# Performance work log

Measured on AMD Instinct MI355X. Metric: run time of the kernel, lower is better.

Reference implementation:

```python
import jax, jax.numpy as jnp
import numpy as np

B, F, S = 64, 128, 2048
K_LIST = [8, 4, 2]  # c**i for i in range(k,0,-1) with k=3, c=2
EPS = 1e-5


def setup_inputs() -> dict:
    key = jax.random.key(0)
    ks = jax.random.split(key, 16)
    d = {}
    d["x"] = jax.random.normal(ks[0], (B, F, S), dtype=jnp.float32)
    # BatchNorm1d(seq_len*feature_num) affine params (train-mode batch stats)
    d["bn_gamma"] = jnp.ones((F * S,), jnp.float32)
    d["bn_beta"] = jnp.zeros((F * S,), jnp.float32)
    i = 1
    for s, k in enumerate(K_LIST):
        L = S // k
        d[f"selw1_{s}"] = (jax.random.normal(ks[i], (3 * F, 64), jnp.float32) / np.sqrt(3 * F)).astype(jnp.float32); i += 1
        d[f"selb1_{s}"] = jnp.zeros((64,), jnp.float32)
        d[f"selw2_{s}"] = (jax.random.normal(ks[i], (64, 1), jnp.float32) / 8.0).astype(jnp.float32); i += 1
        d[f"selb2_{s}"] = jnp.zeros((1,), jnp.float32)
        d[f"linw1_{s}"] = (jax.random.normal(ks[i], (L, L), jnp.float32) / np.sqrt(L)).astype(jnp.float32); i += 1
        d[f"linb1_{s}"] = jnp.zeros((L,), jnp.float32)
        d[f"linw2_{s}"] = (jax.random.normal(ks[i], (L, 2 * L), jnp.float32) / np.sqrt(L)).astype(jnp.float32); i += 1
        d[f"linb2_{s}"] = jnp.zeros((2 * L,), jnp.float32)
    return d


def _forward(x, bn_gamma, bn_beta, sel, lin):
    Bx, Fx, Sx = x.shape
    # BatchNorm1d over flattened [B, F*S] channels, training-mode batch stats (biased var)
    xf = x.reshape(Bx, -1)
    mu = xf.mean(axis=0)
    var = xf.var(axis=0)
    xf = (xf - mu) * jax.lax.rsqrt(var + EPS) * bn_gamma + bn_beta
    x = xf.reshape(Bx, Fx, Sx)

    samples = []
    for s, k in enumerate(K_LIST):
        L = Sx // k
        xr = x.reshape(Bx, Fx, L, k)           # non-overlapping windows (kernel==stride)
        avg = xr.mean(axis=-1)                 # AvgPool1d  [B, F, L]
        mx = xr.max(axis=-1)                   # MaxPool1d  [B, F, L]
        pfs = 0.5 * (avg + mx)
        stats = jnp.concatenate(
            [pfs.mean(axis=-1), pfs.std(axis=-1, ddof=1), pfs.max(axis=-1)], axis=1
        )                                      # [B, 3F]
        w1, b1, w2, b2 = sel[s]
        w = jax.nn.sigmoid(jax.nn.relu(stats @ w1 + b1) @ w2 + b2)  # [B, 1] (dropout is eval/identity)
        w = w[:, :, None]                      # [B, 1, 1]
        samples.append(w * avg + (1.0 - w) * mx)
    samples.append(x)

    for s in range(len(K_LIST)):
        lw1, lb1, lw2, lb2 = lin[s]
        h = jax.nn.gelu(samples[s] @ lw1 + lb1, approximate=False)
        samples[s + 1] = samples[s + 1] + h @ lw2 + lb2
    return samples[-1]


def reference(x, bn_gamma, bn_beta,
              selw1_0, selb1_0, selw2_0, selb2_0, linw1_0, linb1_0, linw2_0, linb2_0,
              selw1_1, selb1_1, selw2_1, selb2_1, linw1_1, linb1_1, linw2_1, linb2_1,
              selw1_2, selb1_2, selw2_2, selb2_2, linw1_2, linb1_2, linw2_2, linb2_2):
    sel = [(selw1_0, selb1_0, selw2_0, selb2_0),
           (selw1_1, selb1_1, selw2_1, selb2_1),
           (selw1_2, selb1_2, selw2_2, selb2_2)]
    lin = [(linw1_0, linb1_0, linw2_0, linb2_0),
           (linw1_1, linb1_1, linw2_1, linb2_1),
           (linw1_2, linb1_2, linw2_2, linb2_2)]
    return _forward(x, bn_gamma, bn_beta, sel, lin)
```

## Files before the change

kernel.cpp:

```cpp
#include <hip/hip_runtime.h>
#include <hip/hip_bf16.h>
#include <math.h>

#define B_ 64
#define F_ 128
#define S_ 2048
#define FS_ (F_*S_)
#define M_  (B_*F_)
#define EPS_ 1e-5f

typedef __bf16 v8bf __attribute__((ext_vector_type(8)));
typedef float  v4f  __attribute__((ext_vector_type(4)));

__device__ __forceinline__ unsigned short f2bf_rne(float f) {
  unsigned int u = __float_as_uint(f);
  u += 0x7FFF + ((u >> 16) & 1);
  return (unsigned short)(u >> 16);
}

__device__ __forceinline__ float gelu_exact(float x) {
  return 0.5f * x * (1.0f + erff(x * 0.70710678118654752f));
}

#define GLDS16(g, l) __builtin_amdgcn_global_load_lds( \
    (const __attribute__((address_space(1))) unsigned int*)(g), \
    (__attribute__((address_space(3))) unsigned int*)(l), 16, 0, 0)

__global__ __launch_bounds__(256) void bn_stats_k(const float* __restrict__ x,
    const float* __restrict__ gamma, const float* __restrict__ beta,
    float* __restrict__ scl, float* __restrict__ shf)
{
  int j4 = blockIdx.x * 256 + threadIdx.x;
  const float4* x4 = (const float4*)x;
  float sum[4] = {0,0,0,0}, sq[4] = {0,0,0,0};
  for (int b = 0; b < B_; b++) {
    float4 v = x4[(size_t)b * (FS_/4) + j4];
    float vv[4] = {v.x, v.y, v.z, v.w};
    #pragma unroll
    for (int i = 0; i < 4; i++) { sum[i] += vv[i]; sq[i] += vv[i]*vv[i]; }
  }
  #pragma unroll
  for (int i = 0; i < 4; i++) {
    int j = j4*4 + i;
    float mu  = sum[i] * (1.0f/B_);
    float var = sq[i] * (1.0f/B_) - mu*mu;
    float rstd = rsqrtf(var + EPS_);
    float g = gamma[j];
    scl[j] = rstd * g;
    shf[j] = beta[j] - mu * rstd * g;
  }
}

__global__ __launch_bounds__(256) void bnpool_k(const float* __restrict__ x,
    const float* __restrict__ scl, const float* __restrict__ shf,
    float* __restrict__ out, float* __restrict__ stats)
{
  int bf = blockIdx.x, t = threadIdx.x;
  int b = bf >> 7, f = bf & 127;
  const float4* xp  = (const float4*)(x   + (size_t)bf * S_);
  const float4* scp = (const float4*)(scl + (size_t)f  * S_);
  const float4* shp = (const float4*)(shf + (size_t)f  * S_);
  float4* op = (float4*)(out + (size_t)bf * S_);

  float xr[8];
  #pragma unroll
  for (int h = 0; h < 2; h++) {
    int i4 = t*2 + h;
    float4 v = xp[i4], sc = scp[i4], sh = shp[i4];
    float4 o;
    o.x = fmaf(v.x, sc.x, sh.x);
    o.y = fmaf(v.y, sc.y, sh.y);
    o.z = fmaf(v.z, sc.z, sh.z);
    o.w = fmaf(v.w, sc.w, sh.w);
    op[i4] = o;
    xr[h*4+0] = o.x; xr[h*4+1] = o.y; xr[h*4+2] = o.z; xr[h*4+3] = o.w;
  }

  float a2[4], m2[4];
  float ps2 = 0.f, pq2 = 0.f, pm2 = -INFINITY;
  #pragma unroll
  for (int j = 0; j < 4; j++) {
    a2[j] = xr[2*j] + xr[2*j+1];
    m2[j] = fmaxf(xr[2*j], xr[2*j+1]);
    float pf = 0.5f * (0.5f * a2[j] + m2[j]);
    ps2 += pf; pq2 += pf*pf; pm2 = fmaxf(pm2, pf);
  }
  float a4[2], m4[2];
  float ps1 = 0.f, pq1 = 0.f, pm1 = -INFINITY;
  #pragma unroll
  for (int j = 0; j < 2; j++) {
    a4[j] = a2[2*j] + a2[2*j+1];
    m4[j] = fmaxf(m2[2*j], m2[2*j+1]);
    float pf = 0.5f * (0.25f * a4[j] + m4[j]);
    ps1 += pf; pq1 += pf*pf; pm1 = fmaxf(pm1, pf);
  }
  float a8 = a4[0] + a4[1];
  float m8 = fmaxf(m4[0], m4[1]);
  float pf8 = 0.5f * (0.125f * a8 + m8);
  float ps0 = pf8, pq0 = pf8*pf8, pm0 = pf8;

  __shared__ float wred[12];
  int lane = t & 63, wid = t >> 6;
  float PS[3] = {ps0, ps1, ps2}, PQ[3] = {pq0, pq1, pq2}, PM[3] = {pm0, pm1, pm2};
  int   LL[3] = {256, 512, 1024};
  #pragma unroll
  for (int s = 0; s < 3; s++) {
    float vs = PS[s], vq = PQ[s], vm = PM[s];
    #pragma unroll
    for (int off = 32; off > 0; off >>= 1) {
      vs += __shfl_down(vs, off);
      vq += __shfl_down(vq, off);
      vm = fmaxf(vm, __shfl_down(vm, off));
    }
    if (lane == 0) { wred[wid*3+0] = vs; wred[wid*3+1] = vq; wred[wid*3+2] = vm; }
    __syncthreads();
    if (t == 0) {
      float S = 0.f, Q = 0.f, Mx = -INFINITY;
      #pragma unroll
      for (int i = 0; i < 4; i++) {
        S += wred[i*3+0]; Q += wred[i*3+1]; Mx = fmaxf(Mx, wred[i*3+2]);
      }
      float L = (float)LL[s];
      float mean = S / L;
      float var  = (Q - S*S/L) / (L - 1.0f);
      float* base = stats + s*(64*384) + b*384;
      base[f]       = mean;
      base[128 + f] = sqrtf(fmaxf(var, 0.0f));
      base[256 + f] = Mx;
    }
    __syncthreads();
  }
}

__global__ __launch_bounds__(64) void selall_k(const float* __restrict__ stats,
    const float* w1_0, const float* b1_0, const float* w2_0, const float* b2_0,
    const float* w1_1, const float* b1_1, const float* w2_1, const float* b2_1,
    const float* w1_2, const float* b1_2, const float* w2_2, const float* b2_2,
    float* __restrict__ wsel)
{
  int s = blockIdx.y, b = blockIdx.x, j = threadIdx.x;
  const float *w1, *b1, *w2, *b2;
  if      (s == 0) { w1 = w1_0; b1 = b1_0; w2 = w2_0; b2 = b2_0; }
  else if (s == 1) { w1 = w1_1; b1 = b1_1; w2 = w2_1; b2 = b2_1; }
  else             { w1 = w1_2; b1 = b1_2; w2 = w2_2; b2 = b2_2; }
  const float* st = stats + s*(64*384) + b*384;
  float acc = b1[j];
  for (int i = 0; i < 384; i++) acc = fmaf(st[i], w1[i*64 + j], acc);
  float h = fmaxf(acc, 0.0f);
  float v = h * w2[j];
  for (int off = 32; off > 0; off >>= 1) v += __shfl_down(v, off);
  if (j == 0) wsel[s*64 + b] = 1.0f / (1.0f + expf(-(v + b2[0])));
}

__global__ __launch_bounds__(256) void combfused_k(const float* __restrict__ xn,
    const float* __restrict__ wsel,
    unsigned short* __restrict__ o8, unsigned short* __restrict__ o4,
    unsigned short* __restrict__ o2)
{
  int bf = blockIdx.x, t = threadIdx.x, b = bf >> 7;
  float wA = wsel[b];
  float wB = wsel[64 + b];
  float wC = wsel[128 + b];
  const float4* xp = (const float4*)(xn + (size_t)bf * S_);
  float xr[8];
  #pragma unroll
  for (int h = 0; h < 2; h++) {
    float4 v = xp[t*2 + h];
    xr[h*4+0] = v.x; xr[h*4+1] = v.y; xr[h*4+2] = v.z; xr[h*4+3] = v.w;
  }
  float a2[4], m2[4];
  ushort4 u4o;
  unsigned short uu[4];
  #pragma unroll
  for (int j = 0; j < 4; j++) {
    a2[j] = xr[2*j] + xr[2*j+1];
    m2[j] = fmaxf(xr[2*j], xr[2*j+1]);
    uu[j] = f2bf_rne(wC * (0.5f * a2[j]) + (1.0f - wC) * m2[j]);
  }
  u4o.x = uu[0]; u4o.y = uu[1]; u4o.z = uu[2]; u4o.w = uu[3];
  ((ushort4*)(o2 + (size_t)bf * 1024))[t] = u4o;

  float a4[2], m4[2];
  ushort2 u2o;
  #pragma unroll
  for (int j = 0; j < 2; j++) {
    a4[j] = a2[2*j] + a2[2*j+1];
    m4[j] = fmaxf(m2[2*j], m2[2*j+1]);
    unsigned short uv = f2bf_rne(wB * (0.25f * a4[j]) + (1.0f - wB) * m4[j]);
    if (j == 0) u2o.x = uv; else u2o.y = uv;
  }
  ((ushort2*)(o4 + (size_t)bf * 512))[t] = u2o;

  float a8 = a4[0] + a4[1];
  float m8 = fmaxf(m4[0], m4[1]);
  o8[(size_t)bf * 256 + t] = f2bf_rne(wA * (0.125f * a8) + (1.0f - wA) * m8);
}

__global__ __launch_bounds__(256) void wt_all_k(
    const float* w10, unsigned short* t10,
    const float* w20, unsigned short* t20,
    const float* w11, unsigned short* t11,
    const float* w21, unsigned short* t21,
    const float* w12, unsigned short* t12,
    const float* w22, unsigned short* t22)
{
  int bx = blockIdx.x;
  const float* W; unsigned short* T; int K, N, loc;
  if      (bx < 64)   { W = w10; T = t10; K = 256;  N = 256;  loc = bx; }
  else if (bx < 192)  { W = w20; T = t20; K = 256;  N = 512;  loc = bx - 64; }
  else if (bx < 448)  { W = w11; T = t11; K = 512;  N = 512;  loc = bx - 192; }
  else if (bx < 960)  { W = w21; T = t21; K = 512;  N = 1024; loc = bx - 448; }
  else if (bx < 1984) { W = w12; T = t12; K = 1024; N = 1024; loc = bx - 960; }
  else                { W = w22; T = t22; K = 1024; N = 2048; loc = bx - 1984; }
  int nx = N >> 5;
  int k0 = (loc / nx) << 5;
  int n0 = (loc % nx) << 5;
  __shared__ float tile[32][33];
  int tx = threadIdx.x & 31, ty = threadIdx.x >> 5;
  #pragma unroll
  for (int i = ty; i < 32; i += 8)
    tile[i][tx] = W[(size_t)(k0 + i) * N + n0 + tx];
  __syncthreads();
  #pragma unroll
  for (int i = ty; i < 32; i += 8)
    T[(size_t)(n0 + i) * K + k0 + tx] = f2bf_rne(tile[tx][i]);
}

template<int MODE>
__global__ __launch_bounds__(256) void mgemm_k(
    const unsigned short* __restrict__ A,
    const unsigned short* __restrict__ Wt,
    const float* __restrict__ bias,
    const float* ColdF,
    const unsigned short* ColdB,
    unsigned short* Obf,
    float* Of32,
    int K, int N)
{
  __shared__ v8bf As8[128*8];
  __shared__ v8bf Bs8[128*8];
  const int tid  = threadIdx.x;
  const int lane = tid & 63;
  const int w    = tid >> 6;
  const int bm   = blockIdx.y * 128;
  const int bn   = blockIdx.x * 128;
  const int wm   = (w >> 1) * 64;
  const int wn   = (w & 1) * 64;

  v4f acc[4][4];
  #pragma unroll
  for (int i = 0; i < 4; i++)
    #pragma unroll
    for (int j = 0; j < 4; j++)
      acc[i][j] = (v4f){0.f, 0.f, 0.f, 0.f};

  const int lrow = lane >> 3;
  const int lchk = (lane & 7) ^ lrow;
  const unsigned short* ag = A  + (size_t)(bm + w*32 + lrow) * K + lchk * 8;
  const unsigned short* bg = Wt + (size_t)(bn + w*32 + lrow) * K + lchk * 8;
  char* al = (char*)As8 + w*32*128;
  char* bl = (char*)Bs8 + w*32*128;
  const size_t row8 = (size_t)8 * K;

  for (int k0 = 0; k0 < K; k0 += 64) {
    __syncthreads();
    GLDS16(ag + k0,            al);
    GLDS16(ag + row8 + k0,     al + 8*128);
    GLDS16(ag + 2*row8 + k0,   al + 16*128);
    GLDS16(ag + 3*row8 + k0,   al + 24*128);
    GLDS16(bg + k0,            bl);
    GLDS16(bg + row8 + k0,     bl + 8*128);
    GLDS16(bg + 2*row8 + k0,   bl + 16*128);
    GLDS16(bg + 3*row8 + k0,   bl + 24*128);
    __syncthreads();

    #pragma unroll
    for (int u = 0; u < 2; u++) {
      const int cl = (lane >> 4) + u*4;
      const int slot = cl ^ (lane & 7);
      v8bf af[4], bfr[4];
      #pragma unroll
      for (int t = 0; t < 4; t++) {
        af[t]  = As8[(wm + t*16 + (lane & 15))*8 + slot];
        bfr[t] = Bs8[(wn + t*16 + (lane & 15))*8 + slot];
      }
      #pragma unroll
      for (int i = 0; i < 4; i++)
        #pragma unroll
        for (int j = 0; j < 4; j++)
          acc[i][j] = __builtin_amdgcn_mfma_f32_16x16x32_bf16(af[i], bfr[j], acc[i][j], 0, 0, 0);
    }
  }

  const int col0 = bn + wn + (lane & 15);
  const int row0 = bm + wm + ((lane >> 4) << 2);
  #pragma unroll
  for (int j = 0; j < 4; j++) {
    int c = col0 + j*16;
    float bv = bias[c];
    #pragma unroll
    for (int i = 0; i < 4; i++) {
      #pragma unroll
      for (int r = 0; r < 4; r++) {
        int rr = row0 + i*16 + r;
        size_t idx = (size_t)rr * N + c;
        float t = acc[i][j][r] + bv;
        if (MODE == 0) {
          Obf[idx] = f2bf_rne(gelu_exact(t));
        } else if (MODE == 1) {
          float cold = __bfloat162float(*(const __hip_bfloat16*)&ColdB[idx]);
          Obf[idx] = f2bf_rne(t + cold);
        } else {
          Of32[idx] = t + ColdF[idx];
        }
      }
    }
  }
}

extern "C" void kernel_launch(void* const* d_in, const int* in_sizes, int n_in,
                              void* d_out, int out_size, void* d_ws, size_t ws_size,
                              hipStream_t stream)
{
  const float* x     = (const float*)d_in[0];
  const float* gamma = (const float*)d_in[1];
  const float* beta  = (const float*)d_in[2];
  float* out = (float*)d_out;
  float* ws  = (float*)d_ws;

  static const int KS[3] = {8, 4, 2};

  size_t off = 0;
  float* scl   = ws + off; off += FS_;
  float* shf   = ws + off; off += FS_;
  float* stats = ws + off; off += 3*64*384;
  float* wsel  = ws + off; off += 256;
  unsigned short* sampb[3];
  sampb[0] = (unsigned short*)(ws + off); off += (size_t)M_ * 256 / 2;
  sampb[1] = (unsigned short*)(ws + off); off += (size_t)M_ * 512 / 2;
  sampb[2] = (unsigned short*)(ws + off); off += (size_t)M_ * 1024 / 2;
  unsigned short* hb = (unsigned short*)(ws + off); off += (size_t)M_ * 2048 / 2;
  unsigned short *wt1[3], *wt2[3];
  for (int s = 0; s < 3; s++) {
    int L = S_ / KS[s];
    wt1[s] = (unsigned short*)(ws + off); off += (size_t)L * L / 2;
    wt2[s] = (unsigned short*)(ws + off); off += (size_t)L * 2 * L / 2;
  }

  wt_all_k<<<4032, 256, 0, stream>>>(
      (const float*)d_in[3 + 0*8 + 4], wt1[0], (const float*)d_in[3 + 0*8 + 6], wt2[0],
      (const float*)d_in[3 + 1*8 + 4], wt1[1], (const float*)d_in[3 + 1*8 + 6], wt2[1],
      (const float*)d_in[3 + 2*8 + 4], wt1[2], (const float*)d_in[3 + 2*8 + 6], wt2[2]);

  bn_stats_k<<<FS_/4/256, 256, 0, stream>>>(x, gamma, beta, scl, shf);
  bnpool_k<<<M_, 256, 0, stream>>>(x, scl, shf, out, stats);
  selall_k<<<dim3(64, 3), 64, 0, stream>>>(stats,
      (const float*)d_in[3+0], (const float*)d_in[4+0], (const float*)d_in[5+0], (const float*)d_in[6+0],
      (const float*)d_in[3+8], (const float*)d_in[4+8], (const float*)d_in[5+8], (const float*)d_in[6+8],
      (const float*)d_in[3+16], (const float*)d_in[4+16], (const float*)d_in[5+16], (const float*)d_in[6+16],
      wsel);
  combfused_k<<<M_, 256, 0, stream>>>(out, wsel, sampb[0], sampb[1], sampb[2]);

  for (int s = 0; s < 3; s++) {
    int L = S_ / KS[s];
    const float* lb1 = (const float*)d_in[3 + 8*s + 5];
    const float* lb2 = (const float*)d_in[3 + 8*s + 7];
    mgemm_k<0><<<dim3(L/128, M_/128), 256, 0, stream>>>(
        sampb[s], wt1[s], lb1, nullptr, nullptr, hb, nullptr, L, L);
    if (s < 2) {
      mgemm_k<1><<<dim3(2*L/128, M_/128), 256, 0, stream>>>(
          hb, wt2[s], lb2, nullptr, sampb[s+1], sampb[s+1], nullptr, L, 2*L);
    } else {
      mgemm_k<2><<<dim3(2*L/128, M_/128), 256, 0, stream>>>(
          hb, wt2[s], lb2, out, nullptr, nullptr, out, L, 2*L);
    }
  }
}
```

Baseline: 412.8 us.

## Store normalized input as bf16 and switch GEMMs to 32x32x16 MFMA tiles

The BN-normalized activation is now written as a bf16 buffer instead of fp32 to the output. The pooling/combine kernel and the final residual GEMM read that buffer, which halves the traffic for the intermediate. The GEMM kernel now uses 32x32x16 bf16 MFMA with a templated M tile (64 for the smaller GEMMs, which gives more blocks) in place of 16x16x32. The risk is that the final residual adds a bf16-rounded x rather than fp32, which lowers accuracy of the output.

```diff
diff --git a/kernel.cpp b/kernel.cpp
--- a/kernel.cpp
+++ b/kernel.cpp
@@ -10,12 +10,18 @@
 #define EPS_ 1e-5f
 
 typedef __bf16 v8bf __attribute__((ext_vector_type(8)));
-typedef float  v4f  __attribute__((ext_vector_type(4)));
+typedef float  v16f __attribute__((ext_vector_type(16)));
 
 __device__ __forceinline__ unsigned short f2bf_rne(float f) {
   unsigned int u = __float_as_uint(f);
   u += 0x7FFF + ((u >> 16) & 1);
   return (unsigned short)(u >> 16);
+}
+__device__ __forceinline__ float b2f(unsigned short u) {
+  return __uint_as_float(((unsigned int)u) << 16);
+}
+__device__ __forceinline__ unsigned int pack2(float a, float b) {
+  return (unsigned int)f2bf_rne(a) | ((unsigned int)f2bf_rne(b) << 16);
 }
 
 __device__ __forceinline__ float gelu_exact(float x) {
@@ -53,28 +59,28 @@
 
 __global__ __launch_bounds__(256) void bnpool_k(const float* __restrict__ x,
     const float* __restrict__ scl, const float* __restrict__ shf,
-    float* __restrict__ out, float* __restrict__ stats)
+    unsigned short* __restrict__ xnb, float* __restrict__ stats)
 {
   int bf = blockIdx.x, t = threadIdx.x;
   int b = bf >> 7, f = bf & 127;
   const float4* xp  = (const float4*)(x   + (size_t)bf * S_);
   const float4* scp = (const float4*)(scl + (size_t)f  * S_);
   const float4* shp = (const float4*)(shf + (size_t)f  * S_);
-  float4* op = (float4*)(out + (size_t)bf * S_);
 
   float xr[8];
   #pragma unroll
   for (int h = 0; h < 2; h++) {
     int i4 = t*2 + h;
     float4 v = xp[i4], sc = scp[i4], sh = shp[i4];
-    float4 o;
-    o.x = fmaf(v.x, sc.x, sh.x);
-    o.y = fmaf(v.y, sc.y, sh.y);
-    o.z = fmaf(v.z, sc.z, sh.z);
-    o.w = fmaf(v.w, sc.w, sh.w);
-    op[i4] = o;
-    xr[h*4+0] = o.x; xr[h*4+1] = o.y; xr[h*4+2] = o.z; xr[h*4+3] = o.w;
-  }
+    xr[h*4+0] = fmaf(v.x, sc.x, sh.x);
+    xr[h*4+1] = fmaf(v.y, sc.y, sh.y);
+    xr[h*4+2] = fmaf(v.z, sc.z, sh.z);
+    xr[h*4+3] = fmaf(v.w, sc.w, sh.w);
+  }
+  uint4 pk;
+  pk.x = pack2(xr[0], xr[1]); pk.y = pack2(xr[2], xr[3]);
+  pk.z = pack2(xr[4], xr[5]); pk.w = pack2(xr[6], xr[7]);
+  ((uint4*)(xnb + (size_t)bf * S_))[t] = pk;
 
   float a2[4], m2[4];
   float ps2 = 0.f, pq2 = 0.f, pm2 = -INFINITY;
@@ -152,7 +158,7 @@
   if (j == 0) wsel[s*64 + b] = 1.0f / (1.0f + expf(-(v + b2[0])));
 }
 
-__global__ __launch_bounds__(256) void combfused_k(const float* __restrict__ xn,
+__global__ __launch_bounds__(256) void combfused_k(const unsigned short* __restrict__ xnb,
     const float* __restrict__ wsel,
     unsigned short* __restrict__ o8, unsigned short* __restrict__ o4,
     unsigned short* __restrict__ o2)
@@ -161,12 +167,13 @@
   float wA = wsel[b];
   float wB = wsel[64 + b];
   float wC = wsel[128 + b];
-  const float4* xp = (const float4*)(xn + (size_t)bf * S_);
+  uint4 pk = ((const uint4*)(xnb + (size_t)bf * S_))[t];
+  unsigned int pw[4] = {pk.x, pk.y, pk.z, pk.w};
   float xr[8];
   #pragma unroll
-  for (int h = 0; h < 2; h++) {
-    float4 v = xp[t*2 + h];
-    xr[h*4+0] = v.x; xr[h*4+1] = v.y; xr[h*4+2] = v.z; xr[h*4+3] = v.w;
+  for (int h = 0; h < 4; h++) {
+    xr[2*h]   = b2f((unsigned short)(pw[h] & 0xFFFF));
+    xr[2*h+1] = b2f((unsigned short)(pw[h] >> 16));
   }
   float a2[4], m2[4];
   ushort4 u4o;
@@ -226,92 +233,92 @@
     T[(size_t)(n0 + i) * K + k0 + tx] = f2bf_rne(tile[tx][i]);
 }
 
-template<int MODE>
+template<int MODE, int TM>
 __global__ __launch_bounds__(256) void mgemm_k(
     const unsigned short* __restrict__ A,
     const unsigned short* __restrict__ Wt,
     const float* __restrict__ bias,
-    const float* ColdF,
-    const unsigned short* ColdB,
+    const unsigned short* Cold,
     unsigned short* Obf,
     float* Of32,
     int K, int N)
 {
-  __shared__ v8bf As8[128*8];
-  __shared__ v8bf Bs8[128*8];
+  constexpr int MI = TM / 64;
+  constexpr int RA = TM / 4;
+  __shared__ v8bf As8[TM * 8];
+  __shared__ v8bf Bs8[128 * 8];
   const int tid  = threadIdx.x;
   const int lane = tid & 63;
   const int w    = tid >> 6;
-  const int bm   = blockIdx.y * 128;
+  const int bm   = blockIdx.y * TM;
   const int bn   = blockIdx.x * 128;
-  const int wm   = (w >> 1) * 64;
+  const int wm   = (w >> 1) * (TM / 2);
   const int wn   = (w & 1) * 64;
 
-  v4f acc[4][4];
-  #pragma unroll
-  for (int i = 0; i < 4; i++)
-    #pragma unroll
-    for (int j = 0; j < 4; j++)
-      acc[i][j] = (v4f){0.f, 0.f, 0.f, 0.f};
+  v16f acc[MI][2];
+  #pragma unroll
+  for (int i = 0; i < MI; i++)
+    #pragma unroll
+    for (int j = 0; j < 2; j++)
+      #pragma unroll
+      for (int r = 0; r < 16; r++) acc[i][j][r] = 0.f;
 
   const int lrow = lane >> 3;
   const int lchk = (lane & 7) ^ lrow;
-  const unsigned short* ag = A  + (size_t)(bm + w*32 + lrow) * K + lchk * 8;
+  const unsigned short* ag = A  + (size_t)(bm + w*RA + lrow) * K + lchk * 8;
   const unsigned short* bg = Wt + (size_t)(bn + w*32 + lrow) * K + lchk * 8;
-  char* al = (char*)As8 + w*32*128;
+  char* al = (char*)As8 + w*RA*128;
   char* bl = (char*)Bs8 + w*32*128;
   const size_t row8 = (size_t)8 * K;
 
   for (int k0 = 0; k0 < K; k0 += 64) {
     __syncthreads();
-    GLDS16(ag + k0,            al);
-    GLDS16(ag + row8 + k0,     al + 8*128);
-    GLDS16(ag + 2*row8 + k0,   al + 16*128);
-    GLDS16(ag + 3*row8 + k0,   al + 24*128);
-    GLDS16(bg + k0,            bl);
-    GLDS16(bg + row8 + k0,     bl + 8*128);
-    GLDS16(bg + 2*row8 + k0,   bl + 16*128);
-    GLDS16(bg + 3*row8 + k0,   bl + 24*128);
+    #pragma unroll
+    for (int q = 0; q < RA/8; q++)
+      GLDS16(ag + q*row8 + k0, al + q*8*128);
+    #pragma unroll
+    for (int q = 0; q < 4; q++)
+      GLDS16(bg + q*row8 + k0, bl + q*8*128);
     __syncthreads();
 
     #pragma unroll
-    for (int u = 0; u < 2; u++) {
-      const int cl = (lane >> 4) + u*4;
-      const int slot = cl ^ (lane & 7);
-      v8bf af[4], bfr[4];
-      #pragma unroll
-      for (int t = 0; t < 4; t++) {
-        af[t]  = As8[(wm + t*16 + (lane & 15))*8 + slot];
-        bfr[t] = Bs8[(wn + t*16 + (lane & 15))*8 + slot];
-      }
-      #pragma unroll
-      for (int i = 0; i < 4; i++)
+    for (int s = 0; s < 4; s++) {
+      const int c = 2*s + (lane >> 5);
+      const int slot = c ^ (lane & 7);
+      v8bf af[MI], bfr[2];
+      #pragma unroll
+      for (int i = 0; i < MI; i++)
+        af[i] = As8[(wm + i*32 + (lane & 31))*8 + slot];
+      #pragma unroll
+      for (int j = 0; j < 2; j++)
+        bfr[j] = Bs8[(wn + j*32 + (lane & 31))*8 + slot];
+      #pragma unroll
+      for (int i = 0; i < MI; i++)
         #pragma unroll
-        for (int j = 0; j < 4; j++)
-          acc[i][j] = __builtin_amdgcn_mfma_f32_16x16x32_bf16(af[i], bfr[j], acc[i][j], 0, 0, 0);
+        for (int j = 0; j < 2; j++)
+          acc[i][j] = __builtin_amdgcn_mfma_f32_32x32x16_bf16(af[i], bfr[j], acc[i][j], 0, 0, 0);
     }
   }
 
-  const int col0 = bn + wn + (lane & 15);
-  const int row0 = bm + wm + ((lane >> 4) << 2);
-  #pragma unroll
-  for (int j = 0; j < 4; j++) {
-    int c = col0 + j*16;
+  const int col0 = bn + wn + (lane & 31);
+  const int rb0  = bm + wm + ((lane >> 5) << 2);
+  #pragma unroll
+  for (int j = 0; j < 2; j++) {
+    int c = col0 + j*32;
     float bv = bias[c];
     #pragma unroll
-    for (int i = 0; i < 4; i++) {
-      #pragma unroll
-      for (int r = 0; r < 4; r++) {
-        int rr = row0 + i*16 + r;
+    for (int i = 0; i < MI; i++) {
+      #pragma unroll
+      for (int r = 0; r < 16; r++) {
+        int rr = rb0 + i*32 + (r & 3) + ((r >> 2) << 3);
         size_t idx = (size_t)rr * N + c;
         float t = acc[i][j][r] + bv;
         if (MODE == 0) {
           Obf[idx] = f2bf_rne(gelu_exact(t));
         } else if (MODE == 1) {
-          float cold = __bfloat162float(*(const __hip_bfloat16*)&ColdB[idx]);
-          Obf[idx] = f2bf_rne(t + cold);
+          Obf[idx] = f2bf_rne(t + b2f(Cold[idx]));
         } else {
-          Of32[idx] = t + ColdF[idx];
+          Of32[idx] = t + b2f(Cold[idx]);
         }
       }
     }
@@ -335,6 +342,7 @@
   float* shf   = ws + off; off += FS_;
   float* stats = ws + off; off += 3*64*384;
   float* wsel  = ws + off; off += 256;
+  unsigned short* xnb = (unsigned short*)(ws + off); off += (size_t)M_ * S_ / 2;
   unsigned short* sampb[3];
   sampb[0] = (unsigned short*)(ws + off); off += (size_t)M_ * 256 / 2;
   sampb[1] = (unsigned short*)(ws + off); off += (size_t)M_ * 512 / 2;
@@ -353,26 +361,24 @@
       (const float*)d_in[3 + 2*8 + 4], wt1[2], (const float*)d_in[3 + 2*8 + 6], wt2[2]);
 
   bn_stats_k<<<FS_/4/256, 256, 0, stream>>>(x, gamma, beta, scl, shf);
-  bnpool_k<<<M_, 256, 0, stream>>>(x, scl, shf, out, stats);
+  bnpool_k<<<M_, 256, 0, stream>>>(x, scl, shf, xnb, stats);
   selall_k<<<dim3(64, 3), 64, 0, stream>>>(stats,
       (const float*)d_in[3+0], (const float*)d_in[4+0], (const float*)d_in[5+0], (const float*)d_in[6+0],
       (const float*)d_in[3+8], (const float*)d_in[4+8], (const float*)d_in[5+8], (const float*)d_in[6+8],
       (const float*)d_in[3+16], (const float*)d_in[4+16], (const float*)d_in[5+16], (const float*)d_in[6+16],
       wsel);
-  combfused_k<<<M_, 256, 0, stream>>>(out, wsel, sampb[0], sampb[1], sampb[2]);
-
-  for (int s = 0; s < 3; s++) {
-    int L = S_ / KS[s];
-    const float* lb1 = (const float*)d_in[3 + 8*s + 5];
-    const float* lb2 = (const float*)d_in[3 + 8*s + 7];
-    mgemm_k<0><<<dim3(L/128, M_/128), 256, 0, stream>>>(
-        sampb[s], wt1[s], lb1, nullptr, nullptr, hb, nullptr, L, L);
-    if (s < 2) {
-      mgemm_k<1><<<dim3(2*L/128, M_/128), 256, 0, stream>>>(
-          hb, wt2[s], lb2, nullptr, sampb[s+1], sampb[s+1], nullptr, L, 2*L);
-    } else {
-      mgemm_k<2><<<dim3(2*L/128, M_/128), 256, 0, stream>>>(
-          hb, wt2[s], lb2, out, nullptr, nullptr, out, L, 2*L);
-    }
-  }
-}
+  combfused_k<<<M_, 256, 0, stream>>>(xnb, wsel, sampb[0], sampb[1], sampb[2]);
+
+  mgemm_k<0,64><<<dim3(2, 128), 256, 0, stream>>>(
+      sampb[0], wt1[0], (const float*)d_in[3+0*8+5], nullptr, hb, nullptr, 256, 256);
+  mgemm_k<1,64><<<dim3(4, 128), 256, 0, stream>>>(
+      hb, wt2[0], (const float*)d_in[3+0*8+7], sampb[1], sampb[1], nullptr, 256, 512);
+  mgemm_k<0,64><<<dim3(4, 128), 256, 0, stream>>>(
+      sampb[1], wt1[1], (const float*)d_in[3+1*8+5], nullptr, hb, nullptr, 512, 512);
+  mgemm_k<1,64><<<dim3(8, 128), 256, 0, stream>>>(
+      hb, wt2[1], (const float*)d_in[3+1*8+7], sampb[2], sampb[2], nullptr, 512, 1024);
+  mgemm_k<0,64><<<dim3(8, 128), 256, 0, stream>>>(
+      sampb[2], wt1[2], (const float*)d_in[3+2*8+5], nullptr, hb, nullptr, 1024, 1024);
+  mgemm_k<2,128><<<dim3(16, 64), 256, 0, stream>>>(
+      hb, wt2[2], (const float*)d_in[3+2*8+7], xnb, nullptr, out, 1024, 2048);
+}
```

After: 372.0 us. 9.9% less time.
